# Optimization experiments

Measured on AMD Instinct MI355X. Metric: run time of the kernel, lower is better.

The kernel has to match this reference:

```python
import jax, jax.numpy as jnp
import numpy as np

N_NODES = 100000


def setup_inputs() -> dict:
    key = jax.random.key(0)
    k1, k2, k3, k4, k5 = jax.random.split(key, 5)
    dim_in, dim_out = 128, 128
    x = jax.random.normal(k1, (N_NODES, dim_in), dtype=jnp.float32)
    edge_index = jax.random.randint(k2, (2, 1600000), 0, N_NODES, dtype=jnp.int64)
    # PyG SAGEConv params: lin_l (neighbor path, with bias), lin_r (root path, no bias)
    s = 1.0 / np.sqrt(dim_in)
    W_l = jax.random.uniform(k3, (dim_in, dim_out), jnp.float32, -s, s)
    b_l = jax.random.uniform(k4, (dim_out,), jnp.float32, -s, s)
    W_r = jax.random.uniform(k5, (dim_in, dim_out), jnp.float32, -s, s)
    return {"x": x, "edge_index": edge_index, "W_l": W_l, "b_l": b_l, "W_r": W_r}


def reference(x, edge_index, W_l, b_l, W_r):
    src, dst = edge_index[0], edge_index[1]
    # mean aggregation of source features onto target nodes
    gathered = x[src]                                   # [E, d_in]
    summed = jax.ops.segment_sum(gathered, dst, num_segments=N_NODES)
    ones = jnp.ones((edge_index.shape[1],), dtype=x.dtype)
    count = jax.ops.segment_sum(ones, dst, num_segments=N_NODES)
    agg = summed / jnp.maximum(count, 1.0)[:, None]     # [N, d_in]
    # out = lin_l(agg) + lin_r(x)
    return agg @ W_l + b_l + x @ W_r
```

## Files before the change

### kernel.cpp

```cpp
#include <hip/hip_runtime.h>

#define N_NODES 100000
#define DIM 128
#define NE 1600000
#define NTILES (N_NODES / 8)
#define GEMM_BLOCKS 2048
#define CHUNK 512
#define NCHUNK ((N_NODES + CHUNK - 1) / CHUNK)

#define WT_BLOCKS 128
#define NCOARSE 391
#define CPAD 16
#define CCAP 4608
#define CB_BLOCKS 512
#define EPA (NE / CB_BLOCKS)
#define BCAP 640
#define NFINE 3125
#define AGG_SPLIT 1563

typedef unsigned short u16;
typedef __attribute__((ext_vector_type(8))) short bf16x8;
typedef __attribute__((ext_vector_type(4))) float f32x4;

__device__ __forceinline__ float bf2f(u16 h) {
  return __uint_as_float(((unsigned int)h) << 16);
}
__device__ __forceinline__ u16 f2bf(float f) {
  unsigned int u = __float_as_uint(f);
  unsigned int lsb = (u >> 16) & 1u;
  u += 0x7fffu + lsb;
  return (u16)(u >> 16);
}


__global__ __launch_bounds__(256) void prep_k(const float* __restrict__ x,
                                              const float* __restrict__ Wl,
                                              const float* __restrict__ Wr,
                                              u16* __restrict__ Ax,
                                              u16* __restrict__ Wt,
                                              int* __restrict__ curC) {
  const int blk = blockIdx.x;
  if (blk < WT_BLOCKS) {
    int idx = blk * 256 + threadIdx.x;
    if (idx < NCOARSE * CPAD) curC[idx] = 0;
    int n = idx >> 8;
    int k = idx & 255;
    float v = (k < 128) ? Wr[(size_t)k * DIM + n] : Wl[(size_t)(k - 128) * DIM + n];
    Wt[(size_t)n * 256 + k] = f2bf(v);
    return;
  }
  int t = (blk - WT_BLOCKS) * 256 + threadIdx.x;
  int row = t >> 5;
  int c = (t & 31) * 4;
  float4 v = *(const float4*)(x + (size_t)row * DIM + c);
  ushort4 o;
  o.x = f2bf(v.x); o.y = f2bf(v.y); o.z = f2bf(v.z); o.w = f2bf(v.w);
  *(ushort4*)(Ax + (size_t)row * DIM + c) = o;
}

__global__ __launch_bounds__(512) void coarse_bin_k(const int* __restrict__ ei,
                                                    int* __restrict__ curC,
                                                    int* __restrict__ binnedC) {
  __shared__ u16 keyS[EPA];
  __shared__ int recS[EPA];
  __shared__ u16 key2[EPA];
  __shared__ int rec2[EPA];
  __shared__ int hist[NCOARSE];
  __shared__ int off[NCOARSE];
  __shared__ int lcur[NCOARSE];
  __shared__ int gbase[NCOARSE];
  const int tid = threadIdx.x;
  const int e0 = blockIdx.x * EPA;

  for (int i = tid; i < NCOARSE; i += 512) hist[i] = 0;
  __syncthreads();
  for (int i = tid; i < EPA; i += 512) {
    int src = ei[e0 + i];
    int dst = ei[NE + e0 + i];
    keyS[i] = (u16)(dst >> 8);
    recS[i] = ((dst & 255) << 17) | src;
    atomicAdd(&hist[dst >> 8], 1);
  }
  __syncthreads();
  if (tid < 64) {
    const int base = tid * 7;
    int h[7];
    int s = 0;
#pragma unroll
    for (int k = 0; k < 7; ++k) {
      int idx = base + k;
      int v = (idx < NCOARSE) ? hist[idx] : 0;
      h[k] = v;
      s += v;
    }
    int sc = s;
    for (int o = 1; o < 64; o <<= 1) {
      int t = __shfl_up(sc, o);
      if (tid >= o) sc += t;
    }
    int ex = sc - s;
#pragma unroll
    for (int k = 0; k < 7; ++k) {
      int idx = base + k;
      if (idx < NCOARSE) {
        off[idx] = ex;
        lcur[idx] = ex;
        gbase[idx] = h[k] ? atomicAdd(&curC[idx * CPAD], h[k]) : 0;
        ex += h[k];
      }
    }
  }
  __syncthreads();
  for (int i = tid; i < EPA; i += 512) {
    int k = keyS[i];
    int p = atomicAdd(&lcur[k], 1);
    rec2[p] = recS[i];
    key2[p] = (u16)k;
  }
  __syncthreads();
  for (int i = tid; i < EPA; i += 512) {
    int k = key2[i];
    int gp = gbase[k] + (i - off[k]);
    if (gp < CCAP) binnedC[(size_t)k * CCAP + gp] = rec2[i];
  }
}

__global__ __launch_bounds__(256) void fine_bin_k(const int* __restrict__ curC,
                                                  const int* __restrict__ binnedC,
                                                  int* __restrict__ binned,
                                                  int* __restrict__ ncnt) {
  __shared__ int recS[CCAP];
  __shared__ int rec2[CCAP];
  __shared__ u16 key2[CCAP];
  __shared__ int hist[256];
  __shared__ int off[256];
  __shared__ int lcur[256];
  __shared__ int foff[8];
  const int c = blockIdx.x;
  const int tid = threadIdx.x;
  int cnt = curC[c * CPAD];
  if (cnt > CCAP) cnt = CCAP;

  hist[tid] = 0;
  __syncthreads();
  for (int i = tid; i < cnt; i += 256) {
    int r = binnedC[(size_t)c * CCAP + i];
    recS[i] = r;
    atomicAdd(&hist[(r >> 17) & 255], 1);
  }
  __syncthreads();
  ncnt[c * 256 + tid] = hist[tid];
  if (tid < 64) {
    int h0 = hist[4 * tid], h1 = hist[4 * tid + 1];
    int h2 = hist[4 * tid + 2], h3 = hist[4 * tid + 3];
    int s = h0 + h1 + h2 + h3;
    int sc = s;
    for (int o = 1; o < 64; o <<= 1) {
      int t = __shfl_up(sc, o);
      if (tid >= o) sc += t;
    }
    int ex = sc - s;
    off[4 * tid] = ex;                lcur[4 * tid] = ex;
    off[4 * tid + 1] = ex + h0;       lcur[4 * tid + 1] = ex + h0;
    off[4 * tid + 2] = ex + h0 + h1;  lcur[4 * tid + 2] = ex + h0 + h1;
    off[4 * tid + 3] = ex + h0 + h1 + h2;
    lcur[4 * tid + 3] = ex + h0 + h1 + h2;
  }
  __syncthreads();
  if (tid < 8) foff[tid] = off[tid * 32];
  __syncthreads();
  for (int i = tid; i < cnt; i += 256) {
    int r = recS[i];
    int p = atomicAdd(&lcur[(r >> 17) & 255], 1);
    rec2[p] = (r & 0x1FFFF) << 7;
    key2[p] = (u16)((r >> 17) & 255);
  }
  __syncthreads();
  for (int i = tid; i < cnt; i += 256) {
    int f = key2[i] >> 5;
    int sl = i - foff[f];
    if (sl < BCAP)
      binned[(size_t)(c * 8 + f) * BCAP + sl] = rec2[i];
  }
}

__global__ __launch_bounds__(256) void aggGemm_k(int base,
                                                 const int* __restrict__ ncnt,
                                                 const int* __restrict__ binned,
                                                 const u16* __restrict__ Ax,
                                                 const u16* __restrict__ Wt,
                                                 const float* __restrict__ bias,
                                                 float* __restrict__ out) {
  __shared__ int srcS[BCAP];
  __shared__ u16 aggS[32][136];
  __shared__ int hist[32];
  __shared__ int off[32];
  __shared__ int cntS;
  const int b = base + blockIdx.x;
  const size_t lo = (size_t)b * BCAP;
  const int nbase = (b >> 3) * 256 + (b & 7) * 32;

  if (threadIdx.x < 32) {
    int d = ncnt[nbase + threadIdx.x];
    hist[threadIdx.x] = d;
    off[threadIdx.x] = d;
  }
  __syncthreads();
  for (int st = 1; st < 32; st <<= 1) {
    int add = 0;
    if (threadIdx.x < 32 && threadIdx.x >= st) add = off[threadIdx.x - st];
    __syncthreads();
    if (threadIdx.x < 32) off[threadIdx.x] += add;
    __syncthreads();
  }
  if (threadIdx.x == 0) cntS = off[31] > BCAP ? BCAP : off[31];
  __syncthreads();
  const int cnt = cntS;
  for (int i = threadIdx.x; i < cnt; i += 256)
    srcS[i] = __builtin_nontemporal_load(&binned[lo + i]);
  __syncthreads();

  const int wave = threadIdx.x >> 6;
  const int lane = threadIdx.x & 63;
  const int half = lane >> 5;
  const int l5 = lane & 31;
  for (int ln = wave; ln < 32; ln += 4) {
    int d = hist[ln];
    int e1 = off[ln];
    if (e1 > cnt) e1 = cnt;
    int j = e1 - d;
    if (j < 0) j = 0;
    float a0 = 0.f, a1 = 0.f, a2 = 0.f, a3 = 0.f;
    for (; j + 4 <= e1; j += 4) {
      int sA = srcS[j + half];
      int sB = srcS[j + 2 + half];
      uint2 uA = *(const uint2*)(Ax + (size_t)(sA + l5 * 4));
      uint2 uB = *(const uint2*)(Ax + (size_t)(sB + l5 * 4));
      a0 += bf2f((u16)uA.x) + bf2f((u16)uB.x);
      a1 += bf2f((u16)(uA.x >> 16)) + bf2f((u16)(uB.x >> 16));
      a2 += bf2f((u16)uA.y) + bf2f((u16)uB.y);
      a3 += bf2f((u16)(uA.y >> 16)) + bf2f((u16)(uB.y >> 16));
    }
    if (j + 2 <= e1) {
      int sA = srcS[j + half];
      uint2 uA = *(const uint2*)(Ax + (size_t)(sA + l5 * 4));
      a0 += bf2f((u16)uA.x);
      a1 += bf2f((u16)(uA.x >> 16));
      a2 += bf2f((u16)uA.y);
      a3 += bf2f((u16)(uA.y >> 16));
      j += 2;
    }
    if (j < e1 && half == 0) {
      int sA = srcS[j];
      uint2 uA = *(const uint2*)(Ax + (size_t)(sA + l5 * 4));
      a0 += bf2f((u16)uA.x);
      a1 += bf2f((u16)(uA.x >> 16));
      a2 += bf2f((u16)uA.y);
      a3 += bf2f((u16)(uA.y >> 16));
    }
    a0 += __shfl_xor(a0, 32);
    a1 += __shfl_xor(a1, 32);
    a2 += __shfl_xor(a2, 32);
    a3 += __shfl_xor(a3, 32);
    if (half == 0) {
      float scale = 1.0f / fmaxf((float)d, 1.0f);
      uint2 pp;
      pp.x = (unsigned)f2bf(a0 * scale) | ((unsigned)f2bf(a1 * scale) << 16);
      pp.y = (unsigned)f2bf(a2 * scale) | ((unsigned)f2bf(a3 * scale) << 16);
      *(uint2*)&((unsigned*)aggS)[ln * 68 + l5 * 2] = pp;
    }
  }
  __syncthreads();

  const int m = lane & 15;
  const int q = lane >> 4;
  const int n0 = wave * 32;
  const float b0 = bias[n0 + m];
  const float b1 = bias[n0 + 16 + m];
  const u16* bp0 = Wt + (size_t)(n0 + m) * 256 + q * 8;
  const u16* bp1 = Wt + (size_t)(n0 + 16 + m) * 256 + q * 8;

#pragma clang loop unroll(disable)
  for (int t = 0; t < 2; ++t) {
    const int row = b * 32 + t * 16 + m;
    f32x4 acc0 = {0.f, 0.f, 0.f, 0.f};
    f32x4 acc1 = {0.f, 0.f, 0.f, 0.f};
    {
      const u16* apx = Ax + (size_t)row * DIM + q * 8;
      bf16x8 A0 = *(const bf16x8*)(apx + 0 * 32);
      bf16x8 A1 = *(const bf16x8*)(apx + 1 * 32);
      bf16x8 A2 = *(const bf16x8*)(apx + 2 * 32);
      bf16x8 A3 = *(const bf16x8*)(apx + 3 * 32);
      acc0 = __builtin_amdgcn_mfma_f32_16x16x32_bf16(A0, *(const bf16x8*)(bp0 + 0 * 32), acc0, 0, 0, 0);
      acc1 = __builtin_amdgcn_mfma_f32_16x16x32_bf16(A0, *(const bf16x8*)(bp1 + 0 * 32), acc1, 0, 0, 0);
      acc0 = __builtin_amdgcn_mfma_f32_16x16x32_bf16(A1, *(const bf16x8*)(bp0 + 1 * 32), acc0, 0, 0, 0);
      acc1 = __builtin_amdgcn_mfma_f32_16x16x32_bf16(A1, *(const bf16x8*)(bp1 + 1 * 32), acc1, 0, 0, 0);
      acc0 = __builtin_amdgcn_mfma_f32_16x16x32_bf16(A2, *(const bf16x8*)(bp0 + 2 * 32), acc0, 0, 0, 0);
      acc1 = __builtin_amdgcn_mfma_f32_16x16x32_bf16(A2, *(const bf16x8*)(bp1 + 2 * 32), acc1, 0, 0, 0);
      acc0 = __builtin_amdgcn_mfma_f32_16x16x32_bf16(A3, *(const bf16x8*)(bp0 + 3 * 32), acc0, 0, 0, 0);
      acc1 = __builtin_amdgcn_mfma_f32_16x16x32_bf16(A3, *(const bf16x8*)(bp1 + 3 * 32), acc1, 0, 0, 0);
    }
    {
      const u16* apg = &aggS[t * 16 + m][q * 8];
      bf16x8 A4 = *(const bf16x8*)(apg + 0 * 32);
      bf16x8 A5 = *(const bf16x8*)(apg + 1 * 32);
      bf16x8 A6 = *(const bf16x8*)(apg + 2 * 32);
      bf16x8 A7 = *(const bf16x8*)(apg + 3 * 32);
      acc0 = __builtin_amdgcn_mfma_f32_16x16x32_bf16(A4, *(const bf16x8*)(bp0 + 4 * 32), acc0, 0, 0, 0);
      acc1 = __builtin_amdgcn_mfma_f32_16x16x32_bf16(A4, *(const bf16x8*)(bp1 + 4 * 32), acc1, 0, 0, 0);
      acc0 = __builtin_amdgcn_mfma_f32_16x16x32_bf16(A5, *(const bf16x8*)(bp0 + 5 * 32), acc0, 0, 0, 0);
      acc1 = __builtin_amdgcn_mfma_f32_16x16x32_bf16(A5, *(const bf16x8*)(bp1 + 5 * 32), acc1, 0, 0, 0);
      acc0 = __builtin_amdgcn_mfma_f32_16x16x32_bf16(A6, *(const bf16x8*)(bp0 + 6 * 32), acc0, 0, 0, 0);
      acc1 = __builtin_amdgcn_mfma_f32_16x16x32_bf16(A6, *(const bf16x8*)(bp1 + 6 * 32), acc1, 0, 0, 0);
      acc0 = __builtin_amdgcn_mfma_f32_16x16x32_bf16(A7, *(const bf16x8*)(bp0 + 7 * 32), acc0, 0, 0, 0);
      acc1 = __builtin_amdgcn_mfma_f32_16x16x32_bf16(A7, *(const bf16x8*)(bp1 + 7 * 32), acc1, 0, 0, 0);
    }
    float* o = out + (size_t)(b * 32 + t * 16 + q * 4) * DIM + n0 + m;
#pragma unroll
    for (int r = 0; r < 4; ++r) {
      __builtin_nontemporal_store(acc0[r] + b0, &o[(size_t)r * DIM]);
      __builtin_nontemporal_store(acc1[r] + b1, &o[(size_t)r * DIM + 16]);
    }
  }
}

__global__ __launch_bounds__(256) void hist_k(const int* __restrict__ ei,
                                              int* __restrict__ deg) {
  int e = blockIdx.x * 256 + threadIdx.x;
  if (e < NE) atomicAdd(&deg[ei[NE + e]], 1);
}

__global__ __launch_bounds__(512) void scan_sum_k(const int* __restrict__ deg,
                                                  int* __restrict__ partials) {
  __shared__ int s[CHUNK];
  int i = blockIdx.x * CHUNK + threadIdx.x;
  s[threadIdx.x] = (i < N_NODES) ? deg[i] : 0;
  __syncthreads();
  for (int off = 256; off > 0; off >>= 1) {
    if (threadIdx.x < off) s[threadIdx.x] += s[threadIdx.x + off];
    __syncthreads();
  }
  if (threadIdx.x == 0) partials[blockIdx.x] = s[0];
}

__global__ __launch_bounds__(256) void scan_part_k(int* __restrict__ partials) {
  __shared__ int s[256];
  int t = threadIdx.x;
  int v = (t < NCHUNK) ? partials[t] : 0;
  s[t] = v;
  __syncthreads();
  for (int off = 1; off < 256; off <<= 1) {
    int add = (t >= off) ? s[t - off] : 0;
    __syncthreads();
    s[t] += add;
    __syncthreads();
  }
  if (t < NCHUNK) partials[t] = s[t] - v;
}

__global__ __launch_bounds__(512) void scan_out_k(const int* __restrict__ deg,
                                                  const int* __restrict__ partials,
                                                  int* __restrict__ offsets,
                                                  int* __restrict__ cursor) {
  __shared__ int s[CHUNK];
  int t = threadIdx.x;
  int i = blockIdx.x * CHUNK + t;
  int v = (i < N_NODES) ? deg[i] : 0;
  s[t] = v;
  __syncthreads();
  for (int off = 1; off < CHUNK; off <<= 1) {
    int add = (t >= off) ? s[t - off] : 0;
    __syncthreads();
    s[t] += add;
    __syncthreads();
  }
  if (i < N_NODES) {
    int excl = partials[blockIdx.x] + s[t] - v;
    offsets[i] = excl;
    cursor[i] = excl;
  }
  if (i == 0) offsets[N_NODES] = NE;
}

__global__ __launch_bounds__(256) void fill_k(const int* __restrict__ ei,
                                              int* __restrict__ cursor,
                                              int* __restrict__ csr) {
  int e = blockIdx.x * 256 + threadIdx.x;
  if (e < NE) {
    int dst = ei[NE + e];
    int pos = atomicAdd(&cursor[dst], 1);
    csr[pos] = ei[e];
  }
}

__global__ __launch_bounds__(256) void agg_f32_k(const int* __restrict__ offsets,
                                                 const int* __restrict__ csr,
                                                 const float* __restrict__ x,
                                                 float* __restrict__ agg) {
  int node = blockIdx.x * 4 + (threadIdx.x >> 6);
  int lane = threadIdx.x & 63;
  int beg = offsets[node], end = offsets[node + 1];
  float ax = 0.f, ay = 0.f;
  int i = beg;
  for (; i + 4 <= end; i += 4) {
    int s0 = csr[i], s1 = csr[i + 1], s2 = csr[i + 2], s3 = csr[i + 3];
    float2 v0 = *(const float2*)(x + (size_t)s0 * DIM + lane * 2);
    float2 v1 = *(const float2*)(x + (size_t)s1 * DIM + lane * 2);
    float2 v2 = *(const float2*)(x + (size_t)s2 * DIM + lane * 2);
    float2 v3 = *(const float2*)(x + (size_t)s3 * DIM + lane * 2);
    ax += v0.x + v1.x + v2.x + v3.x;
    ay += v0.y + v1.y + v2.y + v3.y;
  }
  for (; i < end; ++i) {
    float2 v0 = *(const float2*)(x + (size_t)csr[i] * DIM + lane * 2);
    ax += v0.x;
    ay += v0.y;
  }
  float scale = 1.0f / fmaxf((float)(end - beg), 1.0f);
  float2 r;
  r.x = ax * scale;
  r.y = ay * scale;
  *(float2*)(agg + (size_t)node * DIM + lane * 2) = r;
}

__global__ __launch_bounds__(256) void gemm_xw(const float* __restrict__ x,
                                               const float* __restrict__ W,
                                               const float* __restrict__ b,
                                               float* __restrict__ out) {
  __shared__ float Ws[DIM * DIM];
  for (int i = threadIdx.x; i < DIM * DIM; i += 256) Ws[i] = W[i];
  __syncthreads();
  const int c = threadIdx.x & 127;
  const int half = threadIdx.x >> 7;
  const float bias = b[c];
  for (int tile = blockIdx.x; tile < NTILES; tile += gridDim.x) {
    const int row0 = tile * 8 + half * 4;
    const float* r = x + (size_t)row0 * DIM;
    float a0 = 0.f, a1 = 0.f, a2 = 0.f, a3 = 0.f;
#pragma unroll 8
    for (int k4 = 0; k4 < 32; ++k4) {
      float4 p0 = *(const float4*)(r + 0 * DIM + k4 * 4);
      float4 p1 = *(const float4*)(r + 1 * DIM + k4 * 4);
      float4 p2 = *(const float4*)(r + 2 * DIM + k4 * 4);
      float4 p3 = *(const float4*)(r + 3 * DIM + k4 * 4);
      const float* wp = &Ws[k4 * 4 * DIM + c];
      float w0 = wp[0 * DIM], w1 = wp[1 * DIM], w2 = wp[2 * DIM], w3 = wp[3 * DIM];
      a0 += p0.x * w0 + p0.y * w1 + p0.z * w2 + p0.w * w3;
      a1 += p1.x * w0 + p1.y * w1 + p1.z * w2 + p1.w * w3;
      a2 += p2.x * w0 + p2.y * w1 + p2.z * w2 + p2.w * w3;
      a3 += p3.x * w0 + p3.y * w1 + p3.z * w2 + p3.w * w3;
    }
    out[(size_t)(row0 + 0) * DIM + c] = a0 + bias;
    out[(size_t)(row0 + 1) * DIM + c] = a1 + bias;
    out[(size_t)(row0 + 2) * DIM + c] = a2 + bias;
    out[(size_t)(row0 + 3) * DIM + c] = a3 + bias;
  }
}

__global__ __launch_bounds__(256) void gemm_aw(const float* __restrict__ agg,
                                               const float* __restrict__ W,
                                               float* __restrict__ out) {
  __shared__ float Ws[DIM * DIM];
  for (int i = threadIdx.x; i < DIM * DIM; i += 256) Ws[i] = W[i];
  __syncthreads();
  const int c = threadIdx.x & 127;
  const int half = threadIdx.x >> 7;
  for (int tile = blockIdx.x; tile < NTILES; tile += gridDim.x) {
    const int row0 = tile * 8 + half * 4;
    const float* r = agg + (size_t)row0 * DIM;
    float a0 = 0.f, a1 = 0.f, a2 = 0.f, a3 = 0.f;
#pragma unroll 8
    for (int k4 = 0; k4 < 32; ++k4) {
      float4 p0 = *(const float4*)(r + 0 * DIM + k4 * 4);
      float4 p1 = *(const float4*)(r + 1 * DIM + k4 * 4);
      float4 p2 = *(const float4*)(r + 2 * DIM + k4 * 4);
      float4 p3 = *(const float4*)(r + 3 * DIM + k4 * 4);
      const float* wp = &Ws[k4 * 4 * DIM + c];
      float w0 = wp[0 * DIM], w1 = wp[1 * DIM], w2 = wp[2 * DIM], w3 = wp[3 * DIM];
      a0 += p0.x * w0 + p0.y * w1 + p0.z * w2 + p0.w * w3;
      a1 += p1.x * w0 + p1.y * w1 + p1.z * w2 + p1.w * w3;
      a2 += p2.x * w0 + p2.y * w1 + p2.z * w2 + p2.w * w3;
      a3 += p3.x * w0 + p3.y * w1 + p3.z * w2 + p3.w * w3;
    }
    out[(size_t)(row0 + 0) * DIM + c] += a0;
    out[(size_t)(row0 + 1) * DIM + c] += a1;
    out[(size_t)(row0 + 2) * DIM + c] += a2;
    out[(size_t)(row0 + 3) * DIM + c] += a3;
  }
}

extern "C" void kernel_launch(void* const* d_in, const int* in_sizes, int n_in,
                              void* d_out, int out_size, void* d_ws, size_t ws_size,
                              hipStream_t stream) {
  const float* x  = (const float*)d_in[0];
  const int*   ei = (const int*)d_in[1];
  const float* Wl = (const float*)d_in[2];
  const float* bl = (const float*)d_in[3];
  const float* Wr = (const float*)d_in[4];
  float* out = (float*)d_out;

  u16* Ax       = (u16*)d_ws;
  u16* Ag       = Ax + (size_t)N_NODES * DIM;
  int* binnedC  = (int*)Ag;
  int* binned   = binnedC + (size_t)NCOARSE * CCAP;
  u16* Wt       = Ag + (size_t)N_NODES * DIM;
  int* curC     = (int*)(Wt + 128 * 256);
  int* ncnt     = curC + NCOARSE * CPAD;
  size_t needed = (size_t)N_NODES * DIM * 2 * 2 + 65536 +
                  (NCOARSE * CPAD + NCOARSE * 256) * 4;

  if (ws_size >= needed) {
    hipLaunchKernelGGL(prep_k, dim3(WT_BLOCKS + 12500), dim3(256), 0, stream,
                       x, Wl, Wr, Ax, Wt, curC);
    hipLaunchKernelGGL(coarse_bin_k, dim3(CB_BLOCKS), dim3(512), 0, stream,
                       ei, curC, binnedC);
    hipLaunchKernelGGL(fine_bin_k, dim3(NCOARSE), dim3(256), 0, stream,
                       curC, binnedC, binned, ncnt);
    hipLaunchKernelGGL(aggGemm_k, dim3(AGG_SPLIT), dim3(256), 0, stream,
                       0, ncnt, binned, Ax, Wt, bl, out);
    hipLaunchKernelGGL(aggGemm_k, dim3(NFINE - AGG_SPLIT), dim3(256), 0, stream,
                       AGG_SPLIT, ncnt, binned, Ax, Wt, bl, out);
  } else {
    int* deg2      = (int*)d_ws;
    int* offsets2  = deg2 + N_NODES;
    int* partials2 = offsets2 + 100004;
    int* csr2      = partials2 + 256;
    float* agg     = (float*)(csr2 + NE);
    hipMemsetAsync(deg2, 0, (size_t)N_NODES * sizeof(int), stream);
    hipLaunchKernelGGL(hist_k, dim3((NE + 255) / 256), dim3(256), 0, stream, ei, deg2);
    hipLaunchKernelGGL(scan_sum_k, dim3(NCHUNK), dim3(CHUNK), 0, stream, deg2, partials2);
    hipLaunchKernelGGL(scan_part_k, dim3(1), dim3(256), 0, stream, partials2);
    hipLaunchKernelGGL(scan_out_k, dim3(NCHUNK), dim3(CHUNK), 0, stream,
                       deg2, partials2, offsets2, deg2);
    hipLaunchKernelGGL(fill_k, dim3((NE + 255) / 256), dim3(256), 0, stream,
                       ei, deg2, csr2);
    hipLaunchKernelGGL(agg_f32_k, dim3(N_NODES / 4), dim3(256), 0, stream,
                       offsets2, csr2, x, agg);
    hipLaunchKernelGGL(gemm_xw, dim3(GEMM_BLOCKS), dim3(256), 0, stream,
                       x, Wr, bl, out);
    hipLaunchKernelGGL(gemm_aw, dim3(GEMM_BLOCKS), dim3(256), 0, stream,
                       agg, Wl, out);
  }
}
```

Before: 267.5 us.

## Replace global atomic coarse binning with per-block offset tables and segment gather

The coarse binning kernel no longer reserves space in global bins with atomics. Each block instead writes its locally sorted edges contiguously with nontemporal stores and records per-bin offsets in a u16 table. The fine binning kernel gathers each coarse bin's segments from all 512 blocks using a prefix scan over segment counts, and scatters straight to the final bins without a second shared-memory staging pass. The two aggregation/GEMM launches are merged into one. This removes global atomic contention and a shared staging buffer, but adds many small, uncoalesced per-thread segment reads in the fine binning kernel.

```diff
diff --git a/kernel.cpp b/kernel.cpp
--- a/kernel.cpp
+++ b/kernel.cpp
@@ -10,13 +10,12 @@
 
 #define WT_BLOCKS 128
 #define NCOARSE 391
-#define CPAD 16
+#define OFFW 392
 #define CCAP 4608
 #define CB_BLOCKS 512
 #define EPA (NE / CB_BLOCKS)
 #define BCAP 640
 #define NFINE 3125
-#define AGG_SPLIT 1563
 
 typedef unsigned short u16;
 typedef __attribute__((ext_vector_type(8))) short bf16x8;
@@ -37,12 +36,10 @@
                                               const float* __restrict__ Wl,
                                               const float* __restrict__ Wr,
                                               u16* __restrict__ Ax,
-                                              u16* __restrict__ Wt,
-                                              int* __restrict__ curC) {
+                                              u16* __restrict__ Wt) {
   const int blk = blockIdx.x;
   if (blk < WT_BLOCKS) {
     int idx = blk * 256 + threadIdx.x;
-    if (idx < NCOARSE * CPAD) curC[idx] = 0;
     int n = idx >> 8;
     int k = idx & 255;
     float v = (k < 128) ? Wr[(size_t)k * DIM + n] : Wl[(size_t)(k - 128) * DIM + n];
@@ -59,16 +56,14 @@
 }
 
 __global__ __launch_bounds__(512) void coarse_bin_k(const int* __restrict__ ei,
-                                                    int* __restrict__ curC,
+                                                    u16* __restrict__ offM,
                                                     int* __restrict__ binnedC) {
   __shared__ u16 keyS[EPA];
   __shared__ int recS[EPA];
-  __shared__ u16 key2[EPA];
   __shared__ int rec2[EPA];
   __shared__ int hist[NCOARSE];
   __shared__ int off[NCOARSE];
   __shared__ int lcur[NCOARSE];
-  __shared__ int gbase[NCOARSE];
   const int tid = threadIdx.x;
   const int e0 = blockIdx.x * EPA;
 
@@ -105,49 +100,77 @@
       if (idx < NCOARSE) {
         off[idx] = ex;
         lcur[idx] = ex;
-        gbase[idx] = h[k] ? atomicAdd(&curC[idx * CPAD], h[k]) : 0;
+        offM[(size_t)blockIdx.x * OFFW + idx] = (u16)ex;
         ex += h[k];
       }
     }
   }
   __syncthreads();
   for (int i = tid; i < EPA; i += 512) {
-    int k = keyS[i];
-    int p = atomicAdd(&lcur[k], 1);
+    int p = atomicAdd(&lcur[keyS[i]], 1);
     rec2[p] = recS[i];
-    key2[p] = (u16)k;
-  }
-  __syncthreads();
-  for (int i = tid; i < EPA; i += 512) {
-    int k = key2[i];
-    int gp = gbase[k] + (i - off[k]);
-    if (gp < CCAP) binnedC[(size_t)k * CCAP + gp] = rec2[i];
-  }
-}
-
-__global__ __launch_bounds__(256) void fine_bin_k(const int* __restrict__ curC,
+  }
+  __syncthreads();
+  for (int i = tid; i < EPA; i += 512)
+    __builtin_nontemporal_store(rec2[i], &binnedC[(size_t)blockIdx.x * EPA + i]);
+}
+
+__global__ __launch_bounds__(256) void fine_bin_k(const u16* __restrict__ offM,
                                                   const int* __restrict__ binnedC,
                                                   int* __restrict__ binned,
                                                   int* __restrict__ ncnt) {
   __shared__ int recS[CCAP];
-  __shared__ int rec2[CCAP];
-  __shared__ u16 key2[CCAP];
   __shared__ int hist[256];
   __shared__ int off[256];
   __shared__ int lcur[256];
   __shared__ int foff[8];
+  __shared__ int segoff[CB_BLOCKS];
+  __shared__ int segcnt[CB_BLOCKS];
+  __shared__ int segdst[CB_BLOCKS];
+  __shared__ int totS;
   const int c = blockIdx.x;
   const int tid = threadIdx.x;
-  int cnt = curC[c * CPAD];
-  if (cnt > CCAP) cnt = CCAP;
-
+
+  for (int s = tid; s < CB_BLOCKS; s += 256) {
+    int o0 = offM[(size_t)s * OFFW + c];
+    int o1 = (c == NCOARSE - 1) ? EPA : offM[(size_t)s * OFFW + c + 1];
+    segoff[s] = o0;
+    segcnt[s] = o1 - o0;
+  }
+  __syncthreads();
+  int s0 = segcnt[2 * tid], s1 = segcnt[2 * tid + 1];
+  int pair = s0 + s1;
+  off[tid] = pair;
+  __syncthreads();
+  for (int o = 1; o < 256; o <<= 1) {
+    int add = (tid >= o) ? off[tid - o] : 0;
+    __syncthreads();
+    off[tid] += add;
+    __syncthreads();
+  }
+  int ex = off[tid] - pair;
+  segdst[2 * tid] = ex;
+  segdst[2 * tid + 1] = ex + s0;
+  if (tid == 255) totS = off[255];
+  __syncthreads();
+  int tot = totS;
+  if (tot > CCAP) tot = CCAP;
+
+#pragma unroll
+  for (int ss = 0; ss < 2; ++ss) {
+    int s = 2 * tid + ss;
+    int sc = segcnt[s];
+    int sdst = segdst[s];
+    const int* srcp = binnedC + (size_t)s * EPA + segoff[s];
+    for (int k = 0; k < sc; ++k) {
+      int d = sdst + k;
+      if (d < CCAP) recS[d] = srcp[k];
+    }
+  }
   hist[tid] = 0;
   __syncthreads();
-  for (int i = tid; i < cnt; i += 256) {
-    int r = binnedC[(size_t)c * CCAP + i];
-    recS[i] = r;
-    atomicAdd(&hist[(r >> 17) & 255], 1);
-  }
+  for (int i = tid; i < tot; i += 256)
+    atomicAdd(&hist[(recS[i] >> 17) & 255], 1);
   __syncthreads();
   ncnt[c * 256 + tid] = hist[tid];
   if (tid < 64) {
@@ -159,33 +182,28 @@
       int t = __shfl_up(sc, o);
       if (tid >= o) sc += t;
     }
-    int ex = sc - s;
-    off[4 * tid] = ex;                lcur[4 * tid] = ex;
-    off[4 * tid + 1] = ex + h0;       lcur[4 * tid + 1] = ex + h0;
-    off[4 * tid + 2] = ex + h0 + h1;  lcur[4 * tid + 2] = ex + h0 + h1;
-    off[4 * tid + 3] = ex + h0 + h1 + h2;
-    lcur[4 * tid + 3] = ex + h0 + h1 + h2;
+    int ex2 = sc - s;
+    off[4 * tid] = ex2;                lcur[4 * tid] = ex2;
+    off[4 * tid + 1] = ex2 + h0;       lcur[4 * tid + 1] = ex2 + h0;
+    off[4 * tid + 2] = ex2 + h0 + h1;  lcur[4 * tid + 2] = ex2 + h0 + h1;
+    off[4 * tid + 3] = ex2 + h0 + h1 + h2;
+    lcur[4 * tid + 3] = ex2 + h0 + h1 + h2;
   }
   __syncthreads();
   if (tid < 8) foff[tid] = off[tid * 32];
   __syncthreads();
-  for (int i = tid; i < cnt; i += 256) {
+  for (int i = tid; i < tot; i += 256) {
     int r = recS[i];
-    int p = atomicAdd(&lcur[(r >> 17) & 255], 1);
-    rec2[p] = (r & 0x1FFFF) << 7;
-    key2[p] = (u16)((r >> 17) & 255);
-  }
-  __syncthreads();
-  for (int i = tid; i < cnt; i += 256) {
-    int f = key2[i] >> 5;
-    int sl = i - foff[f];
-    if (sl < BCAP)
-      binned[(size_t)(c * 8 + f) * BCAP + sl] = rec2[i];
-  }
-}
-
-__global__ __launch_bounds__(256) void aggGemm_k(int base,
-                                                 const int* __restrict__ ncnt,
+    int node = (r >> 17) & 255;
+    int p = atomicAdd(&lcur[node], 1);
+    int f = node >> 5;
+    int slot = p - foff[f];
+    if (slot < BCAP)
+      binned[(size_t)(c * 8 + f) * BCAP + slot] = (r & 0x1FFFF) << 7;
+  }
+}
+
+__global__ __launch_bounds__(256) void aggGemm_k(const int* __restrict__ ncnt,
                                                  const int* __restrict__ binned,
                                                  const u16* __restrict__ Ax,
                                                  const u16* __restrict__ Wt,
@@ -196,7 +214,7 @@
   __shared__ int hist[32];
   __shared__ int off[32];
   __shared__ int cntS;
-  const int b = base + blockIdx.x;
+  const int b = blockIdx.x;
   const size_t lo = (size_t)b * BCAP;
   const int nbase = (b >> 3) * 256 + (b & 7) * 32;
 
@@ -502,24 +520,22 @@
   u16* Ax       = (u16*)d_ws;
   u16* Ag       = Ax + (size_t)N_NODES * DIM;
   int* binnedC  = (int*)Ag;
-  int* binned   = binnedC + (size_t)NCOARSE * CCAP;
+  int* binned   = binnedC + (size_t)CB_BLOCKS * EPA;
   u16* Wt       = Ag + (size_t)N_NODES * DIM;
-  int* curC     = (int*)(Wt + 128 * 256);
-  int* ncnt     = curC + NCOARSE * CPAD;
+  u16* offM     = (u16*)(Wt + 128 * 256);
+  int* ncnt     = (int*)(offM + (size_t)CB_BLOCKS * OFFW);
   size_t needed = (size_t)N_NODES * DIM * 2 * 2 + 65536 +
-                  (NCOARSE * CPAD + NCOARSE * 256) * 4;
+                  (size_t)CB_BLOCKS * OFFW * 2 + (size_t)NCOARSE * 256 * 4;
 
   if (ws_size >= needed) {
     hipLaunchKernelGGL(prep_k, dim3(WT_BLOCKS + 12500), dim3(256), 0, stream,
-                       x, Wl, Wr, Ax, Wt, curC);
+                       x, Wl, Wr, Ax, Wt);
     hipLaunchKernelGGL(coarse_bin_k, dim3(CB_BLOCKS), dim3(512), 0, stream,
-                       ei, curC, binnedC);
+                       ei, offM, binnedC);
     hipLaunchKernelGGL(fine_bin_k, dim3(NCOARSE), dim3(256), 0, stream,
-                       curC, binnedC, binned, ncnt);
-    hipLaunchKernelGGL(aggGemm_k, dim3(AGG_SPLIT), dim3(256), 0, stream,
-                       0, ncnt, binned, Ax, Wt, bl, out);
-    hipLaunchKernelGGL(aggGemm_k, dim3(NFINE - AGG_SPLIT), dim3(256), 0, stream,
-                       AGG_SPLIT, ncnt, binned, Ax, Wt, bl, out);
+                       offM, binnedC, binned, ncnt);
+    hipLaunchKernelGGL(aggGemm_k, dim3(NFINE), dim3(256), 0, stream,
+                       ncnt, binned, Ax, Wt, bl, out);
   } else {
     int* deg2      = (int*)d_ws;
     int* offsets2  = deg2 + N_NODES;
```

Result: faster. 236.6 us (-11.5%).
